# Optimization experiments

Measured on AMD Instinct MI355X. Metric: run time of the kernel, lower is better.

## Reference

```python
import jax, jax.numpy as jnp
import numpy as np

N_HEAD = 16  # matches init_kwargs
LN_EPS = 1e-5


def setup_inputs() -> dict:
    key = jax.random.key(0)
    k0, k1, k2 = jax.random.split(key, 3)
    S, B, D = 2048, 2, 1024
    N, Dh = N_HEAD, D // N_HEAD
    h = jax.random.normal(k0, (S, B, D), dtype=jnp.float32)
    # causal mask, True = masked; source's dim==3 branch: shape [qlen, klen, batch]
    causal = jnp.triu(jnp.ones((S, S), dtype=bool), k=1)
    attn_mask = jnp.broadcast_to(causal[:, :, None], (S, S, B))
    W_qkv = jax.random.normal(k1, (D, 3 * N * Dh), dtype=jnp.float32) * (1.0 / np.sqrt(D))
    W_o = jax.random.normal(k2, (N * Dh, D), dtype=jnp.float32) * (1.0 / np.sqrt(N * Dh))
    gamma = jnp.ones((D,), dtype=jnp.float32)
    beta = jnp.zeros((D,), dtype=jnp.float32)
    return {"h": h, "attn_mask": attn_mask, "W_qkv": W_qkv, "W_o": W_o,
            "gamma": gamma, "beta": beta}


def reference(h, attn_mask, W_qkv, W_o, gamma, beta):
    # h: [S, B, D] (seq, batch, d_model) -- Transformer-XL layout
    S, B, D = h.shape
    N = N_HEAD
    Dh = W_o.shape[0] // N
    scale = 1.0 / np.sqrt(Dh)

    qkv = h @ W_qkv                                   # [S, B, 3*N*Dh]
    q, k, v = jnp.split(qkv, 3, axis=-1)
    q = q.reshape(S, B, N, Dh)
    k = k.reshape(S, B, N, Dh)
    v = v.reshape(S, B, N, Dh)

    # attention scores: [i, j, b, n]
    score = jnp.einsum('ibnd,jbnd->ijbn', q, k) * scale
    # mask (dim==3 branch of source): attn_mask [i, j, b] -> [i, j, b, 1]
    score = jnp.where(attn_mask[:, :, :, None], -jnp.inf, score)
    prob = jax.nn.softmax(score, axis=1)              # softmax over key axis j

    attn_vec = jnp.einsum('ijbn,jbnd->ibnd', prob, v).reshape(S, B, N * Dh)
    attn_out = attn_vec @ W_o                         # [S, B, D]

    # residual + LayerNorm (biased variance, like torch.nn.LayerNorm)
    x = h + attn_out
    mu = jnp.mean(x, axis=-1, keepdims=True)
    var = jnp.mean(jnp.square(x - mu), axis=-1, keepdims=True)
    out = (x - mu) * jax.lax.rsqrt(var + LN_EPS) * gamma + beta
    return out
```

## Files before the change

kernel.cpp:

```cpp
#include <hip/hip_runtime.h>

typedef unsigned short u16;
typedef unsigned int u32;
typedef __attribute__((ext_vector_type(8))) __bf16 bf16x8;
typedef __attribute__((ext_vector_type(4))) float f32x4;
typedef __attribute__((ext_vector_type(8))) unsigned short u16x8;
typedef __attribute__((ext_vector_type(4))) unsigned short u16x4;

__device__ __forceinline__ u16 f2bf(float f) {
    u32 u = __builtin_bit_cast(u32, f);
    u += 0x7fffu + ((u >> 16) & 1u);
    return (u16)(u >> 16);
}

__device__ __forceinline__ float fexp2(float x) {
#if __has_builtin(__builtin_amdgcn_exp2f)
    return __builtin_amdgcn_exp2f(x);
#else
    return exp2f(x);
#endif
}

__device__ __forceinline__ float frcp(float x) {
#if __has_builtin(__builtin_amdgcn_rcpf)
    return __builtin_amdgcn_rcpf(x);
#else
    return 1.0f / x;
#endif
}

__global__ __launch_bounds__(256) void conv_h_kernel(const float* __restrict__ h,
                                                     u16* __restrict__ hb) {
    int i = blockIdx.x * 256 + threadIdx.x;
    float4 v = ((const float4*)h)[i];
    u16x4 o = { f2bf(v.x), f2bf(v.y), f2bf(v.z), f2bf(v.w) };
    ((u16x4*)hb)[i] = o;
}

__global__ __launch_bounds__(256) void conv_wt_kernel(const float* __restrict__ W,
                                                      u16* __restrict__ Wt,
                                                      int R, int C,
                                                      int scale_rows, float scale) {
    __shared__ float tile[32][33];
    int t = threadIdx.x;
    int r = t >> 3, c4 = (t & 7) * 4;
    int gx = blockIdx.x * 32, gy = blockIdx.y * 32;
    float4 v = *(const float4*)&W[(size_t)(gy + r) * C + gx + c4];
    tile[r][c4 + 0] = v.x; tile[r][c4 + 1] = v.y;
    tile[r][c4 + 2] = v.z; tile[r][c4 + 3] = v.w;
    __syncthreads();
    float sc = (gx + r < scale_rows) ? scale : 1.0f;
    u16x4 o = { f2bf(tile[c4 + 0][r] * sc), f2bf(tile[c4 + 1][r] * sc),
                f2bf(tile[c4 + 2][r] * sc), f2bf(tile[c4 + 3][r] * sc) };
    *(u16x4*)&Wt[(size_t)(gx + r) * R + gy + c4] = o;
}

template <int MODE>
__global__ __launch_bounds__(256) void gemm_bt_kernel(
        const u16* __restrict__ A, const u16* __restrict__ Bt,
        u16* __restrict__ Cb, const float* __restrict__ H, float* __restrict__ X,
        int M, int N, int K) {
    constexpr int LDT = 40;
    __shared__ u16 alds[2][128 * LDT];
    __shared__ u16 blds[2][128 * LDT];
    const int t = threadIdx.x;
    const int lane = t & 63;
    const int wave = t >> 6;
    const int wm = wave >> 1, wn = wave & 1;
    const int m0 = blockIdx.x * 128;
    const int n0 = blockIdx.y * 128;
    const int nk = K >> 5;

    const int srow = t >> 1;
    const int sch = (t & 1) * 2;
    const u16* ga = A + (size_t)(m0 + srow) * K + sch * 8;
    const u16* gb = Bt + (size_t)(n0 + srow) * K + sch * 8;
    const int wo = srow * LDT + sch * 8;

    u16x8 ra0 = *(const u16x8*)(ga);
    u16x8 ra1 = *(const u16x8*)(ga + 8);
    u16x8 rb0 = *(const u16x8*)(gb);
    u16x8 rb1 = *(const u16x8*)(gb + 8);
    *(u16x8*)&alds[0][wo] = ra0;  *(u16x8*)&alds[0][wo + 8] = ra1;
    *(u16x8*)&blds[0][wo] = rb0;  *(u16x8*)&blds[0][wo + 8] = rb1;

    f32x4 acc[4][4] = {};
    const int ko = (lane >> 4) * 8;
    const int arow_base = wm * 64 + (lane & 15);
    const int brow_base = wn * 64 + (lane & 15);

    int cur = 0;
    for (int kt = 0; kt < nk; ++kt) {
        __syncthreads();
        if (kt + 1 < nk) {
            const u16* gan = ga + (kt + 1) * 32;
            const u16* gbn = gb + (kt + 1) * 32;
            ra0 = *(const u16x8*)(gan);
            ra1 = *(const u16x8*)(gan + 8);
            rb0 = *(const u16x8*)(gbn);
            rb1 = *(const u16x8*)(gbn + 8);
        }
        bf16x8 afrag[4], bfrag[4];
#pragma unroll
        for (int m = 0; m < 4; ++m)
            afrag[m] = *(const bf16x8*)&alds[cur][(arow_base + m * 16) * LDT + ko];
#pragma unroll
        for (int n = 0; n < 4; ++n)
            bfrag[n] = *(const bf16x8*)&blds[cur][(brow_base + n * 16) * LDT + ko];
#pragma unroll
        for (int m = 0; m < 4; ++m)
#pragma unroll
            for (int n = 0; n < 4; ++n)
                acc[m][n] = __builtin_amdgcn_mfma_f32_16x16x32_bf16(afrag[m], bfrag[n],
                                                                   acc[m][n], 0, 0, 0);
        if (kt + 1 < nk) {
            *(u16x8*)&alds[cur ^ 1][wo] = ra0;  *(u16x8*)&alds[cur ^ 1][wo + 8] = ra1;
            *(u16x8*)&blds[cur ^ 1][wo] = rb0;  *(u16x8*)&blds[cur ^ 1][wo + 8] = rb1;
        }
        cur ^= 1;
    }

#pragma unroll
    for (int m = 0; m < 4; ++m)
#pragma unroll
        for (int n = 0; n < 4; ++n)
#pragma unroll
            for (int r = 0; r < 4; ++r) {
                int row = m0 + wm * 64 + m * 16 + (lane >> 4) * 4 + r;
                int col = n0 + wn * 64 + n * 16 + (lane & 15);
                size_t idx = (size_t)row * N + col;
                if (MODE == 0) Cb[idx] = f2bf(acc[m][n][r]);
                else           X[idx] = acc[m][n][r] + H[idx];
            }
}

__global__ __launch_bounds__(256) void transpose_v_kernel(const u16* __restrict__ qkvb,
                                                          u16* __restrict__ vt) {
    __shared__ u16 tl[64][72];
    const int t = threadIdx.x;
    const int p = blockIdx.y;
    const int nn = p >> 1, b = p & 1;
    const int s0 = blockIdx.x * 64;
    const int r = t >> 2;
    const int ch = (t & 3) * 2;
    const u16* g = qkvb + ((size_t)(s0 + r) * 2 + b) * 3072 + 2048 + nn * 64;
    *(u16x8*)&tl[r][ch * 8]     = *(const u16x8*)(g + ch * 8);
    *(u16x8*)&tl[r][ch * 8 + 8] = *(const u16x8*)(g + ch * 8 + 8);
    __syncthreads();
    const int dh = t >> 2;
    const int sc = (t & 3) * 2;
    u16* o = vt + ((size_t)p * 64 + dh) * 2048 + s0;
#pragma unroll
    for (int q = 0; q < 2; ++q) {
        int scq = sc + q;
        u16x8 v;
#pragma unroll
        for (int j = 0; j < 8; ++j) v[j] = tl[scq * 8 + j][dh];
        *(u16x8*)(o + scq * 8) = v;
    }
}

__global__ __launch_bounds__(256) void attn_kernel(const u16* __restrict__ qkvb,
                                                   const u16* __restrict__ vt,
                                                   u16* __restrict__ attnb) {
    constexpr int LKT = 72;
    __shared__ u16 klds[64 * LKT];
    __shared__ u16 vlds[64 * LKT];
    __shared__ u16 plds[4][16 * LKT];
    const int t = threadIdx.x;
    const int lane = t & 63;
    const int w = t >> 6;
    const int bid = blockIdx.x;
    const int qt = 31 - (bid >> 5);
    const int p = bid & 31;
    const int nn = p >> 1, b = p & 1;
    const int i0 = qt * 64;

    const int li = lane & 15;
    const int lg = lane >> 4;

    const int qrow = i0 + w * 16 + li;
    const u16* qg = qkvb + ((size_t)qrow * 2 + b) * 3072 + nn * 64 + lg * 8;
    bf16x8 qa0 = *(const bf16x8*)(qg);
    bf16x8 qa1 = *(const bf16x8*)(qg + 32);

    f32x4 o[4] = {};
    float mrun = -3.0e38f;
    float lrun = 0.f;

    const int srow = t >> 2;
    const int sch = (t & 3) * 2;
    const u16* kg = qkvb + 1024 + nn * 64 + sch * 8;
    const u16* vg = vt + ((size_t)p * 64 + srow) * 2048 + sch * 8;

    const int nt = qt + 1;
    u16x8 k0, k1, v0, v1;
    {
        const u16* kgp = kg + ((size_t)srow * 2 + b) * 3072;
        k0 = *(const u16x8*)(kgp);  k1 = *(const u16x8*)(kgp + 8);
        v0 = *(const u16x8*)(vg);   v1 = *(const u16x8*)(vg + 8);
    }
    for (int jt = 0; jt < nt; ++jt) {
        const int j0 = jt * 64;
        __syncthreads();
        *(u16x8*)&klds[srow * LKT + sch * 8] = k0;
        *(u16x8*)&klds[srow * LKT + sch * 8 + 8] = k1;
        *(u16x8*)&vlds[srow * LKT + sch * 8] = v0;
        *(u16x8*)&vlds[srow * LKT + sch * 8 + 8] = v1;
        if (jt + 1 < nt) {
            const u16* kgp = kg + ((size_t)(j0 + 64 + srow) * 2 + b) * 3072;
            k0 = *(const u16x8*)(kgp);  k1 = *(const u16x8*)(kgp + 8);
            const u16* vgp = vg + j0 + 64;
            v0 = *(const u16x8*)(vgp);  v1 = *(const u16x8*)(vgp + 8);
        }
        __syncthreads();

        f32x4 st[4];
#pragma unroll
        for (int cf = 0; cf < 4; ++cf) {
            bf16x8 kb0 = *(const bf16x8*)&klds[(cf * 16 + li) * LKT + lg * 8];
            bf16x8 kb1 = *(const bf16x8*)&klds[(cf * 16 + li) * LKT + 32 + lg * 8];
            f32x4 z = {};
            z = __builtin_amdgcn_mfma_f32_16x16x32_bf16(kb0, qa0, z, 0, 0, 0);
            z = __builtin_amdgcn_mfma_f32_16x16x32_bf16(kb1, qa1, z, 0, 0, 0);
            st[cf] = z;
        }

        if (jt == qt) {
            const int it = w * 16 + li;
#pragma unroll
            for (int cf = 0; cf < 4; ++cf)
#pragma unroll
                for (int r = 0; r < 4; ++r) {
                    int jl = cf * 16 + lg * 4 + r;
                    if (jl > it) st[cf][r] = -3.0e38f;
                }
        }

        float mloc = st[0][0];
#pragma unroll
        for (int cf = 0; cf < 4; ++cf)
#pragma unroll
            for (int r = 0; r < 4; ++r) mloc = fmaxf(mloc, st[cf][r]);
        mloc = fmaxf(mloc, __shfl_xor(mloc, 16, 64));
        mloc = fmaxf(mloc, __shfl_xor(mloc, 32, 64));

        if (__any(mloc > mrun + 8.0f)) {
            float mnew = fmaxf(mrun, mloc);
            float alpha = fexp2(mrun - mnew);
            lrun *= alpha;
            mrun = mnew;
#pragma unroll
            for (int r = 0; r < 4; ++r) {
                float ar = __shfl(alpha, lg * 4 + r, 64);
#pragma unroll
                for (int cf = 0; cf < 4; ++cf) o[cf][r] *= ar;
            }
        }

        float rsum = 0.f;
#pragma unroll
        for (int cf = 0; cf < 4; ++cf) {
            u16x4 pw;
#pragma unroll
            for (int r = 0; r < 4; ++r) {
                float pv = fexp2(st[cf][r] - mrun);
                rsum += pv;
                pw[r] = f2bf(pv);
            }
            *(u16x4*)&plds[w][li * LKT + cf * 16 + lg * 4] = pw;
        }
        rsum += __shfl_xor(rsum, 16, 64);
        rsum += __shfl_xor(rsum, 32, 64);
        lrun += rsum;

        asm volatile("s_waitcnt lgkmcnt(0)" ::: "memory");
        __builtin_amdgcn_sched_barrier(0);

#pragma unroll
        for (int ks = 0; ks < 2; ++ks) {
            bf16x8 pa = *(const bf16x8*)&plds[w][li * LKT + ks * 32 + lg * 8];
#pragma unroll
            for (int cf = 0; cf < 4; ++cf) {
                bf16x8 vb = *(const bf16x8*)&vlds[(cf * 16 + li) * LKT + ks * 32 + lg * 8];
                o[cf] = __builtin_amdgcn_mfma_f32_16x16x32_bf16(pa, vb, o[cf], 0, 0, 0);
            }
        }
    }

    float rinv = frcp(lrun);
#pragma unroll
    for (int r = 0; r < 4; ++r) {
        float rv = __shfl(rinv, lg * 4 + r, 64);
        int srowg = i0 + w * 16 + lg * 4 + r;
        u16* og = attnb + ((size_t)srowg * 2 + b) * 1024 + nn * 64;
#pragma unroll
        for (int cf = 0; cf < 4; ++cf)
            og[cf * 16 + li] = f2bf(o[cf][r] * rv);
    }
}

__global__ __launch_bounds__(256) void ln_kernel(const float* __restrict__ X,
                                                 const float* __restrict__ gamma,
                                                 const float* __restrict__ beta,
                                                 float* __restrict__ out) {
    __shared__ float red[8];
    const int t = threadIdx.x;
    const int row = blockIdx.x;
    float4 v = ((const float4*)(X + (size_t)row * 1024))[t];
    float s = v.x + v.y + v.z + v.w;
#pragma unroll
    for (int off = 1; off < 64; off <<= 1) s += __shfl_xor(s, off, 64);
    if ((t & 63) == 0) red[t >> 6] = s;
    __syncthreads();
    float mu = (red[0] + red[1] + red[2] + red[3]) * (1.f / 1024.f);
    float dx = v.x - mu, dy = v.y - mu, dz = v.z - mu, dw = v.w - mu;
    float q = dx * dx + dy * dy + dz * dz + dw * dw;
#pragma unroll
    for (int off = 1; off < 64; off <<= 1) q += __shfl_xor(q, off, 64);
    if ((t & 63) == 0) red[4 + (t >> 6)] = q;
    __syncthreads();
    float var = (red[4] + red[5] + red[6] + red[7]) * (1.f / 1024.f);
    float rs = rsqrtf(var + 1e-5f);
    float4 g = ((const float4*)gamma)[t];
    float4 bt = ((const float4*)beta)[t];
    float4 o;
    o.x = dx * rs * g.x + bt.x;
    o.y = dy * rs * g.y + bt.y;
    o.z = dz * rs * g.z + bt.z;
    o.w = dw * rs * g.w + bt.w;
    ((float4*)(out + (size_t)row * 1024))[t] = o;
}

extern "C" void kernel_launch(void* const* d_in, const int* in_sizes, int n_in,
                              void* d_out, int out_size, void* d_ws, size_t ws_size,
                              hipStream_t stream) {
    const float* h     = (const float*)d_in[0];
    const float* Wqkv  = (const float*)d_in[2];
    const float* Wo    = (const float*)d_in[3];
    const float* gamma = (const float*)d_in[4];
    const float* beta  = (const float*)d_in[5];
    float* out = (float*)d_out;

    char* ws = (char*)d_ws;
    u16*   hb    = (u16*)(ws);
    u16*   wqkvt = (u16*)(ws + 8388608);
    u16*   wot   = (u16*)(ws + 14680064);
    u16*   qkvb  = (u16*)(ws + 16777216);
    u16*   vt    = (u16*)(ws + 41943040);
    u16*   attnb = (u16*)(ws + 50331648);
    float* xbuf  = (float*)(ws + 58720256);

    const float qscale = 0.125f * 1.44269504088896f;

    conv_h_kernel<<<4096, 256, 0, stream>>>(h, hb);
    conv_wt_kernel<<<dim3(96, 32), 256, 0, stream>>>(Wqkv, wqkvt, 1024, 3072, 1024, qscale);
    conv_wt_kernel<<<dim3(32, 32), 256, 0, stream>>>(Wo, wot, 1024, 1024, 0, 1.0f);
    gemm_bt_kernel<0><<<dim3(32, 24), 256, 0, stream>>>(hb, wqkvt, qkvb, nullptr, nullptr,
                                                        4096, 3072, 1024);
    transpose_v_kernel<<<dim3(32, 32), 256, 0, stream>>>(qkvb, vt);
    attn_kernel<<<1024, 256, 0, stream>>>(qkvb, vt, attnb);
    gemm_bt_kernel<1><<<dim3(32, 8), 256, 0, stream>>>(attnb, wot, nullptr, h, xbuf,
                                                       4096, 1024, 1024);
    ln_kernel<<<4096, 256, 0, stream>>>(xbuf, gamma, beta, out);
}
```

Measured before the change: 122.7 us.

## Use direct global-to-LDS loads in GEMM and permlane P-transpose in attention

The GEMM's staging through registers and padded LDS stores is replaced with global_load_lds DMA writes into an unpadded LDS tile, removing VGPR traffic and LDS store instructions. The cost is possible LDS bank conflicts, since the padding is gone. In attention, the P tile moves from the softmax layout to the MFMA A-operand layout with permlane32/16 swaps and packed bf16 converts instead of an LDS round trip. A permuted query-tile order also balances causal work across CUs. The GEMM loop now waits on vmcnt(0) every iteration, which may limit how much load and compute overlap.

```diff
diff --git a/kernel.cpp b/kernel.cpp
--- a/kernel.cpp
+++ b/kernel.cpp
@@ -6,6 +6,17 @@
 typedef __attribute__((ext_vector_type(4))) float f32x4;
 typedef __attribute__((ext_vector_type(8))) unsigned short u16x8;
 typedef __attribute__((ext_vector_type(4))) unsigned short u16x4;
+typedef __attribute__((ext_vector_type(2))) unsigned int u32x2;
+typedef __attribute__((ext_vector_type(4))) unsigned int u32x4;
+
+#if defined(__has_builtin)
+#if __has_builtin(__builtin_amdgcn_permlane32_swap) && __has_builtin(__builtin_amdgcn_permlane16_swap)
+#define USE_PERMLANE 1
+#endif
+#endif
+#ifndef USE_PERMLANE
+#define USE_PERMLANE 0
+#endif
 
 __device__ __forceinline__ u16 f2bf(float f) {
     u32 u = __builtin_bit_cast(u32, f);
@@ -28,6 +39,10 @@
     return 1.0f / x;
 #endif
 }
+
+#define GLOAD_LDS16(gp, lp) __builtin_amdgcn_global_load_lds(                    \
+    (const __attribute__((address_space(1))) void*)(gp),                          \
+    (__attribute__((address_space(3))) void*)(lp), 16, 0, 0)
 
 __global__ __launch_bounds__(256) void conv_h_kernel(const float* __restrict__ h,
                                                      u16* __restrict__ hb) {
@@ -60,63 +75,62 @@
         const u16* __restrict__ A, const u16* __restrict__ Bt,
         u16* __restrict__ Cb, const float* __restrict__ H, float* __restrict__ X,
         int M, int N, int K) {
-    constexpr int LDT = 40;
-    __shared__ u16 alds[2][128 * LDT];
-    __shared__ u16 blds[2][128 * LDT];
+    __shared__ u16 alds[2][128 * 32];
+    __shared__ u16 blds[2][128 * 32];
     const int t = threadIdx.x;
     const int lane = t & 63;
     const int wave = t >> 6;
     const int wm = wave >> 1, wn = wave & 1;
+    const int li = lane & 15, lg = lane >> 4;
     const int m0 = blockIdx.x * 128;
     const int n0 = blockIdx.y * 128;
     const int nk = K >> 5;
 
-    const int srow = t >> 1;
-    const int sch = (t & 1) * 2;
-    const u16* ga = A + (size_t)(m0 + srow) * K + sch * 8;
-    const u16* gb = Bt + (size_t)(n0 + srow) * K + sch * 8;
-    const int wo = srow * LDT + sch * 8;
-
-    u16x8 ra0 = *(const u16x8*)(ga);
-    u16x8 ra1 = *(const u16x8*)(ga + 8);
-    u16x8 rb0 = *(const u16x8*)(gb);
-    u16x8 rb1 = *(const u16x8*)(gb + 8);
-    *(u16x8*)&alds[0][wo] = ra0;  *(u16x8*)&alds[0][wo + 8] = ra1;
-    *(u16x8*)&blds[0][wo] = rb0;  *(u16x8*)&blds[0][wo + 8] = rb1;
+    const int srow0 = (lane >> 2);
+    const int scol = (lane & 3) * 8;
+    const u16* gA = A + (size_t)(m0 + srow0) * K + scol;
+    const u16* gB = Bt + (size_t)(n0 + srow0) * K + scol;
+
+#define GEMM_STAGE(cur, kt)                                                      \
+    {                                                                            \
+        _Pragma("unroll")                                                        \
+        for (int jj = 0; jj < 2; ++jj) {                                         \
+            const int instr = wave * 2 + jj;                                     \
+            GLOAD_LDS16(gA + (size_t)(instr * 16) * K + (kt) * 32,               \
+                        &alds[cur][instr * 512]);                                \
+            GLOAD_LDS16(gB + (size_t)(instr * 16) * K + (kt) * 32,               \
+                        &blds[cur][instr * 512]);                                \
+        }                                                                        \
+    }
+
+    GEMM_STAGE(0, 0);
 
     f32x4 acc[4][4] = {};
-    const int ko = (lane >> 4) * 8;
-    const int arow_base = wm * 64 + (lane & 15);
-    const int brow_base = wn * 64 + (lane & 15);
+    const int ko = lg * 8;
+    const int arow_base = wm * 64 + li;
+    const int brow_base = wn * 64 + li;
+
+    asm volatile("s_waitcnt vmcnt(0)" ::: "memory");
+    __syncthreads();
 
     int cur = 0;
     for (int kt = 0; kt < nk; ++kt) {
-        __syncthreads();
-        if (kt + 1 < nk) {
-            const u16* gan = ga + (kt + 1) * 32;
-            const u16* gbn = gb + (kt + 1) * 32;
-            ra0 = *(const u16x8*)(gan);
-            ra1 = *(const u16x8*)(gan + 8);
-            rb0 = *(const u16x8*)(gbn);
-            rb1 = *(const u16x8*)(gbn + 8);
-        }
+        if (kt + 1 < nk) GEMM_STAGE(cur ^ 1, kt + 1);
         bf16x8 afrag[4], bfrag[4];
 #pragma unroll
         for (int m = 0; m < 4; ++m)
-            afrag[m] = *(const bf16x8*)&alds[cur][(arow_base + m * 16) * LDT + ko];
+            afrag[m] = *(const bf16x8*)&alds[cur][(arow_base + m * 16) * 32 + ko];
 #pragma unroll
         for (int n = 0; n < 4; ++n)
-            bfrag[n] = *(const bf16x8*)&blds[cur][(brow_base + n * 16) * LDT + ko];
+            bfrag[n] = *(const bf16x8*)&blds[cur][(brow_base + n * 16) * 32 + ko];
 #pragma unroll
         for (int m = 0; m < 4; ++m)
 #pragma unroll
             for (int n = 0; n < 4; ++n)
                 acc[m][n] = __builtin_amdgcn_mfma_f32_16x16x32_bf16(afrag[m], bfrag[n],
                                                                    acc[m][n], 0, 0, 0);
-        if (kt + 1 < nk) {
-            *(u16x8*)&alds[cur ^ 1][wo] = ra0;  *(u16x8*)&alds[cur ^ 1][wo + 8] = ra1;
-            *(u16x8*)&blds[cur ^ 1][wo] = rb0;  *(u16x8*)&blds[cur ^ 1][wo + 8] = rb1;
-        }
+        asm volatile("s_waitcnt vmcnt(0)" ::: "memory");
+        __syncthreads();
         cur ^= 1;
     }
 
@@ -126,8 +140,8 @@
         for (int n = 0; n < 4; ++n)
 #pragma unroll
             for (int r = 0; r < 4; ++r) {
-                int row = m0 + wm * 64 + m * 16 + (lane >> 4) * 4 + r;
-                int col = n0 + wn * 64 + n * 16 + (lane & 15);
+                int row = m0 + wm * 64 + m * 16 + lg * 4 + r;
+                int col = n0 + wn * 64 + n * 16 + li;
                 size_t idx = (size_t)row * N + col;
                 if (MODE == 0) Cb[idx] = f2bf(acc[m][n][r]);
                 else           X[idx] = acc[m][n][r] + H[idx];
@@ -166,12 +180,17 @@
     constexpr int LKT = 72;
     __shared__ u16 klds[64 * LKT];
     __shared__ u16 vlds[64 * LKT];
+#if !USE_PERMLANE
     __shared__ u16 plds[4][16 * LKT];
+#endif
     const int t = threadIdx.x;
     const int lane = t & 63;
     const int w = t >> 6;
     const int bid = blockIdx.x;
-    const int qt = 31 - (bid >> 5);
+    const int g = bid >> 5;
+    const int sq = g & 7, jq = g >> 3;
+    const int qt = (jq == 0) ? (31 - sq) : (jq == 1) ? (16 + sq)
+                 : (jq == 2) ? (15 - sq) : sq;
     const int p = bid & 31;
     const int nn = p >> 1, b = p & 1;
     const int i0 = qt * 64;
@@ -258,6 +277,39 @@
             }
         }
 
+#if USE_PERMLANE
+        float rsum = 0.f;
+        u32 wv[4][2];
+#pragma unroll
+        for (int cf = 0; cf < 4; ++cf)
+#pragma unroll
+            for (int rr = 0; rr < 2; ++rr) {
+                float p0 = fexp2(st[cf][2 * rr] - mrun);
+                float p1 = fexp2(st[cf][2 * rr + 1] - mrun);
+                rsum += p0 + p1;
+                u32 wres;
+                asm("v_cvt_pk_bf16_f32 %0, %1, %2" : "=v"(wres) : "v"(p0), "v"(p1));
+                wv[cf][rr] = wres;
+            }
+        rsum += __shfl_xor(rsum, 16, 64);
+        rsum += __shfl_xor(rsum, 32, 64);
+        lrun += rsum;
+
+#pragma unroll
+        for (int ks = 0; ks < 2; ++ks) {
+            u32x2 sa = __builtin_amdgcn_permlane32_swap(wv[2 * ks][0], wv[2 * ks + 1][0], false, false);
+            u32x2 fa = __builtin_amdgcn_permlane16_swap(sa[0], sa[1], false, false);
+            u32x2 sb = __builtin_amdgcn_permlane32_swap(wv[2 * ks][1], wv[2 * ks + 1][1], false, false);
+            u32x2 fb = __builtin_amdgcn_permlane16_swap(sb[0], sb[1], false, false);
+            u32x4 fw = { fa[0], fb[0], fa[1], fb[1] };
+            bf16x8 pa = __builtin_bit_cast(bf16x8, fw);
+#pragma unroll
+            for (int cf = 0; cf < 4; ++cf) {
+                bf16x8 vb = *(const bf16x8*)&vlds[(cf * 16 + li) * LKT + ks * 32 + lg * 8];
+                o[cf] = __builtin_amdgcn_mfma_f32_16x16x32_bf16(pa, vb, o[cf], 0, 0, 0);
+            }
+        }
+#else
         float rsum = 0.f;
 #pragma unroll
         for (int cf = 0; cf < 4; ++cf) {
@@ -286,6 +338,7 @@
                 o[cf] = __builtin_amdgcn_mfma_f32_16x16x32_bf16(pa, vb, o[cf], 0, 0, 0);
             }
         }
+#endif
     }
 
     float rinv = frcp(lrun);
```

Measured after the change: 123.1 us. Within noise of the previous version (+0.3%).
